# Kernel optimization log

Hardware: AMD Instinct MI355X
Metric: run time of the kernel (lower is better)

## Reference

```python
import jax, jax.numpy as jnp
import numpy as np

B, L, D, H = 2, 2048, 1024, 16
DH = D // H  # per-head dim = 64


def setup_inputs() -> dict:
    key = jax.random.key(0)
    ks = jax.random.split(key, 7)
    s = 1.0 / np.sqrt(D)
    x = jax.random.normal(ks[0], (B, L, D), dtype=jnp.float32)
    Wq = jax.random.normal(ks[1], (D, D), dtype=jnp.float32) * s
    bq = jax.random.normal(ks[2], (D,), dtype=jnp.float32) * s
    Wk = jax.random.normal(ks[3], (D, D), dtype=jnp.float32) * s
    bk = jax.random.normal(ks[4], (D,), dtype=jnp.float32) * s
    Wv = jax.random.normal(ks[5], (D, D), dtype=jnp.float32) * s
    bv = jax.random.normal(ks[6], (D,), dtype=jnp.float32) * s
    # strict upper-triangular causal mask; mask==1 means position is masked (-inf)
    atten_mask = jnp.triu(jnp.ones((L, L), dtype=jnp.int32), k=1)
    return {"x": x, "atten_mask": atten_mask, "Wq": Wq, "bq": bq,
            "Wk": Wk, "bk": bk, "Wv": Wv, "bv": bv}


def reference(x, atten_mask, Wq, bq, Wk, bk, Wv, bv):
    # nn.Linear: y = x @ W^T + b
    q = x @ Wq.T + bq  # [B,L,D]
    k = x @ Wk.T + bk
    v = x @ Wv.T + bv
    # contiguous split into heads == reshape to [B,L,H,DH]
    q = q.reshape(B, L, H, DH)
    k = k.reshape(B, L, H, DH)
    v = v.reshape(B, L, H, DH)
    scale = jnp.sqrt(jnp.float32(DH))
    scores = jnp.einsum('blhd,bmhd->bhlm', q, k) / scale  # [B,H,L,L]
    # torch.where(mask == 1, -inf, scores)
    scores = jnp.where(atten_mask[None, None] == 1, -jnp.inf, scores)
    attn = jax.nn.softmax(scores, axis=-1)
    out = jnp.einsum('bhlm,bmhd->blhd', attn, v)  # [B,L,H,DH]
    return out.reshape(B, L, D)  # concat heads along channel dim
```

## Files before the change

### kernel.cpp

```cpp
#include <hip/hip_runtime.h>
#include <hip/hip_bf16.h>

#define BDIM 2
#define LSEQ 2048
#define DMODEL 1024
#define NH 16
#define DHEAD 64
#define SP 72
#define CTS 136

typedef __bf16 bf16_t;
typedef __attribute__((ext_vector_type(8))) __bf16 bf16x8;
typedef __attribute__((ext_vector_type(4))) __bf16 bf16x4;
typedef __attribute__((ext_vector_type(2))) __bf16 bf16x2;
typedef __attribute__((ext_vector_type(4))) float f32x4;
typedef __attribute__((ext_vector_type(4))) int i32x4;

static __device__ __forceinline__ f32x4 mfma16(bf16x8 a, bf16x8 b, f32x4 c) {
    return __builtin_amdgcn_mfma_f32_16x16x32_bf16(a, b, c, 0, 0, 0);
}

static __device__ __forceinline__ void load_lds16(const bf16_t* g, void* l) {
    __builtin_amdgcn_global_load_lds(
        (const __attribute__((address_space(1))) void*)g,
        (__attribute__((address_space(3))) void*)l, 16, 0, 0);
}

__global__ void convert_all(
    const float* __restrict__ x,
    const float* __restrict__ Wq, const float* __restrict__ Wk, const float* __restrict__ Wv,
    const float* __restrict__ bq, const float* __restrict__ bk, const float* __restrict__ bv,
    bf16_t* __restrict__ cx,
    bf16_t* __restrict__ cWq, bf16_t* __restrict__ cWk, bf16_t* __restrict__ cWv,
    bf16_t* __restrict__ cbq, bf16_t* __restrict__ cbk, bf16_t* __restrict__ cbv,
    float SQ)
{
    const int blk = blockIdx.x;
    const float* src; bf16_t* dst; int base, cnt; float sc = 1.0f;
    if (blk < 1024)      { src = x;  dst = cx;  base = blk * 1024;          cnt = 1024; }
    else if (blk < 1280) { src = Wq; dst = cWq; base = (blk - 1024) * 1024; cnt = 1024; sc = SQ; }
    else if (blk < 1536) { src = Wk; dst = cWk; base = (blk - 1280) * 1024; cnt = 1024; }
    else if (blk < 1792) { src = Wv; dst = cWv; base = (blk - 1536) * 1024; cnt = 1024; }
    else if (blk == 1792){ src = bq; dst = cbq; base = 0; cnt = 256; sc = SQ; }
    else if (blk == 1793){ src = bk; dst = cbk; base = 0; cnt = 256; }
    else                 { src = bv; dst = cbv; base = 0; cnt = 256; }

    for (int i = base + threadIdx.x; i < base + cnt; i += 256) {
        f32x4 v = *(const f32x4*)(src + 4 * (size_t)i);
        bf16x4 o;
        o[0] = (bf16_t)(v[0] * sc); o[1] = (bf16_t)(v[1] * sc);
        o[2] = (bf16_t)(v[2] * sc); o[3] = (bf16_t)(v[3] * sc);
        *(bf16x4*)(dst + 4 * (size_t)i) = o;
    }
}

__global__ __launch_bounds__(256) void qkv_gemm(
    const bf16_t* __restrict__ x,
    const bf16_t* __restrict__ W0, const bf16_t* __restrict__ W1, const bf16_t* __restrict__ W2,
    const bf16_t* __restrict__ b0, const bf16_t* __restrict__ b1, const bf16_t* __restrict__ b2,
    bf16_t* __restrict__ yq, bf16_t* __restrict__ yk, bf16_t* __restrict__ yvT)
{
    __shared__ alignas(16) bf16_t smem[2 * 16384];
    bf16_t* Ct = smem;

    const int tid  = threadIdx.x;
    const int lane = tid & 63;
    const int w    = tid >> 6;
    const int quad = lane >> 4;
    const int n16  = lane & 15;

    const int m0 = blockIdx.y * 128;
    const int n0 = blockIdx.x * 128;
    const int z  = blockIdx.z;

    const bf16_t* W    = (z == 0) ? W0 : ((z == 1) ? W1 : W2);
    const bf16_t* bias = (z == 0) ? b0 : ((z == 1) ? b1 : b2);

    const int wm = (w >> 1) * 64;
    const int wn = (w & 1) * 64;

    f32x4 acc[4][4] = {};

    const int srow  = lane >> 3;
    const int schnk = (lane & 7) ^ srow;
    const bf16_t* gx = x + (size_t)(m0 + w * 32 + srow) * DMODEL + schnk * 8;
    const bf16_t* gw = W + (size_t)(n0 + w * 32 + srow) * DMODEL + schnk * 8;
    const int dOff = w * 2048;

    const int swz = n16 & 7;

    {
        bf16_t* lA = smem + dOff;
        bf16_t* lB = smem + 8192 + dOff;
        #pragma unroll
        for (int ii = 0; ii < 4; ++ii) {
            load_lds16(gx + (size_t)(8 * ii) * DMODEL, lA + ii * 512);
            load_lds16(gw + (size_t)(8 * ii) * DMODEL, lB + ii * 512);
        }
    }
    __syncthreads();

    int buf = 0;
    for (int it = 0; it < 16; ++it) {
        if (it + 1 < 16) {
            const int k0 = (it + 1) * 64;
            bf16_t* lA = smem + (buf ^ 1) * 16384 + dOff;
            bf16_t* lB = smem + (buf ^ 1) * 16384 + 8192 + dOff;
            #pragma unroll
            for (int ii = 0; ii < 4; ++ii) {
                load_lds16(gx + (size_t)(8 * ii) * DMODEL + k0, lA + ii * 512);
                load_lds16(gw + (size_t)(8 * ii) * DMODEL + k0, lB + ii * 512);
            }
        }

        const bf16_t* Ab = smem + buf * 16384;
        const bf16_t* Bb = smem + buf * 16384 + 8192;
        #pragma unroll
        for (int kk = 0; kk < 2; ++kk) {
            bf16x8 af[4], bfv[4];
            #pragma unroll
            for (int mt = 0; mt < 4; ++mt) {
                const bf16_t* ar = Ab + (wm + mt * 16 + n16) * 64;
                af[mt] = *(const bf16x8*)(ar + ((quad + 4 * kk) ^ swz) * 8);
            }
            #pragma unroll
            for (int nt = 0; nt < 4; ++nt) {
                const bf16_t* br = Bb + (wn + nt * 16 + n16) * 64;
                bfv[nt] = *(const bf16x8*)(br + ((quad + 4 * kk) ^ swz) * 8);
            }
            #pragma unroll
            for (int mt = 0; mt < 4; ++mt)
                #pragma unroll
                for (int nt = 0; nt < 4; ++nt)
                    acc[mt][nt] = mfma16(af[mt], bfv[nt], acc[mt][nt]);
        }

        __syncthreads();
        buf ^= 1;
    }

    if (z < 2) {
        bf16_t* y = (z == 0) ? yq : yk;
        #pragma unroll
        for (int nt = 0; nt < 4; ++nt) {
            int jc = wn + nt * 16 + n16;
            float bv = (float)bias[n0 + jc];
            #pragma unroll
            for (int mt = 0; mt < 4; ++mt) {
                int rr = wm + mt * 16 + quad * 4;
                #pragma unroll
                for (int r = 0; r < 4; ++r)
                    Ct[(rr + r) * CTS + jc] = (bf16_t)(acc[mt][nt][r] + bv);
            }
        }
        __syncthreads();
        const int l    = tid >> 1;
        const int half = tid & 1;
        const int hh   = (n0 >> 6) + half;
        const int i    = m0 + l;
        const int bb   = i >> 11, ll = i & 2047;
        bf16_t* dst = &y[(((size_t)bb * NH + hh) * LSEQ + ll) * DHEAD];
        const bf16_t* srcr = &Ct[l * CTS + half * 64];
        #pragma unroll
        for (int c = 0; c < 8; ++c)
            *(bf16x8*)(dst + c * 8) = *(const bf16x8*)(srcr + c * 8);
    } else {
        #pragma unroll
        for (int nt = 0; nt < 4; ++nt) {
            int j = n0 + wn + nt * 16 + n16;
            float bv = (float)bias[j];
            #pragma unroll
            for (int mt = 0; mt < 4; ++mt) {
                int i0 = m0 + wm + mt * 16 + quad * 4;
                int bb = i0 >> 11, l = i0 & 2047;
                bf16x4 pk;
                #pragma unroll
                for (int r = 0; r < 4; ++r) pk[r] = (bf16_t)(acc[mt][nt][r] + bv);
                *(bf16x4*)(&yvT[((size_t)bb * DMODEL + j) * LSEQ + l]) = pk;
            }
        }
    }
}

__global__ __launch_bounds__(256) void attn_fused(
    const bf16_t* __restrict__ qp,
    const bf16_t* __restrict__ kp,
    const bf16_t* __restrict__ vtp,
    float* __restrict__ out,
    float* __restrict__ Opart,
    float* __restrict__ ml)
{
    __shared__ alignas(16) bf16_t Ks[2][64 * 64];
    __shared__ alignas(16) bf16_t Vs[2][64 * 64];
    __shared__ alignas(16) bf16_t Pw[4][2][32 * SP];

    const int tid  = threadIdx.x;
    const int lane = tid & 63;
    const int w    = tid >> 6;
    const int quad = lane >> 4;
    const int n16  = lane & 15;
    const int lane3 = lane >> 3;
    const int lane7 = lane & 7;
    const int swz8  = (lane7 ^ lane3) * 8;
    const int swz   = n16 & 7;

    const int bh  = blockIdx.x;
    const int yy  = blockIdx.y;
    const int p   = yy & 7;
    const bool isA = (yy < 8);
    const int b = bh >> 4, h = bh & 15;
    const size_t hb = (size_t)bh * (LSEQ * DHEAD);

    float l_[2];
    f32x4 oacc[2][4];

    auto process = [&](int qt, int t0, int ntiles, bool maskTail) {
        int iqg[2];
        bf16x8 qb[2][2];
        #pragma unroll
        for (int g = 0; g < 2; ++g) {
            iqg[g] = qt * 128 + 32 * w + 16 * g + n16;
            const bf16_t* qq = qp + hb + (size_t)iqg[g] * DHEAD;
            qb[g][0] = *(const bf16x8*)(qq + quad * 8);
            qb[g][1] = *(const bf16x8*)(qq + 32 + quad * 8);
        }

        const bf16_t* gk = kp  + hb + (size_t)(t0 * 64 + 16 * w + lane3) * DHEAD + swz8;
        const bf16_t* gv = vtp + hb + (size_t)(16 * w + lane3) * LSEQ + t0 * 64 + swz8;

        int buf = 0;
        {
            char* lk = (char*)&Ks[0][0] + w * 2048;
            char* lv = (char*)&Vs[0][0] + w * 2048;
            load_lds16(gk,             lk);
            load_lds16(gk + 8 * DHEAD, lk + 1024);
            load_lds16(gv,             lv);
            load_lds16(gv + 8 * LSEQ,  lv + 1024);
            gk += 64 * DHEAD; gv += 64;
        }
        __syncthreads();

        for (int it = 0; it < ntiles; ++it) {
            if (it + 1 < ntiles) {
                char* lk = (char*)&Ks[buf ^ 1][0] + w * 2048;
                char* lv = (char*)&Vs[buf ^ 1][0] + w * 2048;
                load_lds16(gk,             lk);
                load_lds16(gk + 8 * DHEAD, lk + 1024);
                load_lds16(gv,             lv);
                load_lds16(gv + 8 * LSEQ,  lv + 1024);
                gk += 64 * DHEAD; gv += 64;
            }

            const bf16_t* kb = &Ks[buf][0];
            f32x4 s[2][4];
            #pragma unroll
            for (int t = 0; t < 4; ++t) {
                const bf16_t* krow = kb + (t * 16 + n16) * 64;
                bf16x8 k0v = *(const bf16x8*)(krow + ((quad    ) ^ swz) * 8);
                bf16x8 k1v = *(const bf16x8*)(krow + ((quad + 4) ^ swz) * 8);
                #pragma unroll
                for (int g = 0; g < 2; ++g) {
                    f32x4 z = {0.f, 0.f, 0.f, 0.f};
                    z = mfma16(k0v, qb[g][0], z);
                    z = mfma16(k1v, qb[g][1], z);
                    s[g][t] = z;
                }
            }

            if (maskTail && it >= ntiles - 2) {
                const int k0 = (t0 + it) * 64;
                #pragma unroll
                for (int g = 0; g < 2; ++g)
                    #pragma unroll
                    for (int t = 0; t < 4; ++t)
                        #pragma unroll
                        for (int r = 0; r < 4; ++r)
                            if (k0 + t * 16 + quad * 4 + r > iqg[g]) s[g][t][r] = -1e30f;
            }

            #pragma unroll
            for (int g = 0; g < 2; ++g) {
                bf16_t* pw = &Pw[w][buf][g * 16 * SP] + n16 * SP + quad * 4;
                float rs = 0.f;
                #pragma unroll
                for (int t = 0; t < 4; ++t) {
                    float p0 = __builtin_amdgcn_exp2f(s[g][t][0]);
                    float p1 = __builtin_amdgcn_exp2f(s[g][t][1]);
                    float p2 = __builtin_amdgcn_exp2f(s[g][t][2]);
                    float p3 = __builtin_amdgcn_exp2f(s[g][t][3]);
                    rs += (p0 + p1) + (p2 + p3);
                    bf16x4 pk;
                    pk[0] = (bf16_t)p0; pk[1] = (bf16_t)p1;
                    pk[2] = (bf16_t)p2; pk[3] = (bf16_t)p3;
                    *(bf16x4*)(pw + t * 16) = pk;
                }
                l_[g] += rs;
            }

            asm volatile("s_waitcnt lgkmcnt(0)" ::: "memory");

            const bf16_t* vbs = &Vs[buf][0];
            #pragma unroll
            for (int c = 0; c < 2; ++c) {
                bf16x8 pb0 = *(const bf16x8*)(&Pw[w][buf][0]       + n16 * SP + c * 32 + quad * 8);
                bf16x8 pb1 = *(const bf16x8*)(&Pw[w][buf][16 * SP] + n16 * SP + c * 32 + quad * 8);
                #pragma unroll
                for (int t = 0; t < 4; ++t) {
                    const bf16_t* vrow = vbs + (t * 16 + n16) * 64;
                    bf16x8 va = *(const bf16x8*)(vrow + ((quad + 4 * c) ^ swz) * 8);
                    oacc[0][t] = mfma16(va, pb0, oacc[0][t]);
                    oacc[1][t] = mfma16(va, pb1, oacc[1][t]);
                }
            }

            __syncthreads();
            buf ^= 1;
        }
    };

    auto zero_state = [&]() {
        #pragma unroll
        for (int g = 0; g < 2; ++g) {
            l_[g] = 0.f;
            #pragma unroll
            for (int t = 0; t < 4; ++t) { f32x4 zz = {0.f,0.f,0.f,0.f}; oacc[g][t] = zz; }
        }
    };

    auto store_partial = [&](int pidx) {
        #pragma unroll
        for (int g = 0; g < 2; ++g) {
            float ls = l_[g];
            ls += __shfl_xor(ls, 16, 64);
            ls += __shfl_xor(ls, 32, 64);
            const int row = 32 * w + 16 * g + n16;
            float* Ob = Opart + (size_t)pidx * (128 * 64) + row * 64;
            #pragma unroll
            for (int t = 0; t < 4; ++t)
                *(f32x4*)(Ob + t * 16 + quad * 4) = oacc[g][t];
            if (quad == 0) ml[(size_t)pidx * 128 + row] = ls;
        }
    };

    if (isA) {
        zero_state();
        process(p, 0, 2 * p + 2, true);
        #pragma unroll
        for (int g = 0; g < 2; ++g) {
            float ls = l_[g];
            ls += __shfl_xor(ls, 16, 64);
            ls += __shfl_xor(ls, 32, 64);
            const float inv = 1.0f / ls;
            const int iq = p * 128 + 32 * w + 16 * g + n16;
            float* orow = out + ((size_t)b * LSEQ + iq) * DMODEL + h * DHEAD;
            #pragma unroll
            for (int t = 0; t < 4; ++t) {
                f32x4 o;
                o[0] = oacc[g][t][0] * inv; o[1] = oacc[g][t][1] * inv;
                o[2] = oacc[g][t][2] * inv; o[3] = oacc[g][t][3] * inv;
                *(f32x4*)(orow + t * 16 + quad * 4) = o;
            }
        }
        zero_state();
        process(15 - p, 0, 15 - 2 * p, false);
        store_partial((bh * 8 + (7 - p)) * 2 + 0);
    } else {
        zero_state();
        process(15 - p, 15 - 2 * p, 17, true);
        store_partial((bh * 8 + (7 - p)) * 2 + 1);
    }
}

__global__ __launch_bounds__(256) void attn_combine(
    const float* __restrict__ Opart, const float* __restrict__ ml,
    float* __restrict__ out)
{
    const int bh = blockIdx.x;
    const int q8 = blockIdx.y;
    const int t  = threadIdx.x;
    const int row = t >> 1;
    const int dh0 = (t & 1) * 32;
    const int p0  = (bh * 8 + q8) * 2;
    const int b = bh >> 4, h = bh & 15;

    float l0 = ml[(size_t)p0 * 128 + row];
    float l1 = ml[(size_t)(p0 + 1) * 128 + row];
    float inv = 1.0f / (l0 + l1);

    const float* P0 = Opart + (size_t)p0 * (128 * 64) + row * 64 + dh0;
    const float* P1 = P0 + 128 * 64;
    float* orow = out + ((size_t)b * LSEQ + ((8 + q8) * 128 + row)) * DMODEL
                + h * DHEAD + dh0;
    #pragma unroll
    for (int c = 0; c < 8; ++c) {
        f32x4 o0 = *(const f32x4*)(P0 + 4 * c);
        f32x4 o1 = *(const f32x4*)(P1 + 4 * c);
        f32x4 o;
        o[0] = (o0[0] + o1[0]) * inv;
        o[1] = (o0[1] + o1[1]) * inv;
        o[2] = (o0[2] + o1[2]) * inv;
        o[3] = (o0[3] + o1[3]) * inv;
        *(f32x4*)(orow + 4 * c) = o;
    }
}

extern "C" void kernel_launch(void* const* d_in, const int* in_sizes, int n_in,
                              void* d_out, int out_size, void* d_ws, size_t ws_size,
                              hipStream_t stream)
{
    const float* x  = (const float*)d_in[0];
    const float* Wq = (const float*)d_in[2];
    const float* bq = (const float*)d_in[3];
    const float* Wk = (const float*)d_in[4];
    const float* bk = (const float*)d_in[5];
    const float* Wv = (const float*)d_in[6];
    const float* bv = (const float*)d_in[7];
    float* out = (float*)d_out;

    char* ws = (char*)d_ws;
    bf16_t* q   = (bf16_t*)(ws);
    bf16_t* k   = (bf16_t*)(ws + 8u  * 1024 * 1024);
    bf16_t* vT  = (bf16_t*)(ws + 16u * 1024 * 1024);
    bf16_t* cx  = (bf16_t*)(ws + 24u * 1024 * 1024);
    bf16_t* cWq = (bf16_t*)(ws + 32u * 1024 * 1024);
    bf16_t* cWk = (bf16_t*)(ws + 34u * 1024 * 1024);
    bf16_t* cWv = (bf16_t*)(ws + 36u * 1024 * 1024);
    bf16_t* cbq = (bf16_t*)(ws + 38u * 1024 * 1024);
    bf16_t* cbk = (bf16_t*)(ws + 38u * 1024 * 1024 + 4096);
    bf16_t* cbv = (bf16_t*)(ws + 38u * 1024 * 1024 + 8192);
    float*  mlp = (float*) (ws + 39u * 1024 * 1024);
    float*  Op  = (float*) (ws + 40u * 1024 * 1024);

    const float SQ = 0.125f * 1.44269504088896f;

    convert_all<<<1795, 256, 0, stream>>>(x, Wq, Wk, Wv, bq, bk, bv,
                                          cx, cWq, cWk, cWv, cbq, cbk, cbv, SQ);

    dim3 g1(DMODEL / 128, (BDIM * LSEQ) / 128, 3);
    qkv_gemm<<<g1, 256, 0, stream>>>(cx, cWq, cWk, cWv, cbq, cbk, cbv, q, k, vT);

    dim3 g2(BDIM * NH, 16, 1);
    attn_fused<<<g2, 256, 0, stream>>>(q, k, vT, out, Op, mlp);

    dim3 g3(BDIM * NH, 8, 1);
    attn_combine<<<g3, 256, 0, stream>>>(Op, mlp, out);
}
```

Before: 174.8 us.

## Restructure QKV GEMM into 256x256 tiles with 8 waves and interleaved async staging

The QKV projection GEMM moves from 128x128 tiles with 4 waves to 256x256 tiles with 8 waves and 128KB of LDS. The k-loop is split into quarter phases that interleave global-to-LDS loads for the next A tile and the B tile two steps ahead with MFMA bursts. These phases use explicit barriers, waitcnt, sched_barrier and setprio. The grid shrinks to 192 blocks with a swizzled tile order for L2 locality. This targets more operand reuse per LDS load and better memory/compute overlap, at the cost of fewer blocks on the GPU and tricky hand synchronisation.

```diff
diff --git a/kernel.cpp b/kernel.cpp
--- a/kernel.cpp
+++ b/kernel.cpp
@@ -54,125 +54,167 @@
     }
 }
 
-__global__ __launch_bounds__(256) void qkv_gemm(
+__global__ __launch_bounds__(512, 2) void qkv_gemm(
     const bf16_t* __restrict__ x,
     const bf16_t* __restrict__ W0, const bf16_t* __restrict__ W1, const bf16_t* __restrict__ W2,
     const bf16_t* __restrict__ b0, const bf16_t* __restrict__ b1, const bf16_t* __restrict__ b2,
     bf16_t* __restrict__ yq, bf16_t* __restrict__ yk, bf16_t* __restrict__ yvT)
 {
-    __shared__ alignas(16) bf16_t smem[2 * 16384];
-    bf16_t* Ct = smem;
+    __shared__ alignas(16) bf16_t smem[65536];
 
     const int tid  = threadIdx.x;
     const int lane = tid & 63;
     const int w    = tid >> 6;
     const int quad = lane >> 4;
     const int n16  = lane & 15;
-
-    const int m0 = blockIdx.y * 128;
-    const int n0 = blockIdx.x * 128;
-    const int z  = blockIdx.z;
+    const int swz  = n16 & 7;
+    const int srow = lane >> 3;
+    const int schnk = (lane & 7) ^ srow;
+
+    const int s   = blockIdx.x;
+    const int sem = ((s & 7) << 3) | (s >> 3);
+    const int m0  = (sem >> 2) * 256;
+    const int n0  = (sem & 3) * 256;
+    const int z   = blockIdx.y;
 
     const bf16_t* W    = (z == 0) ? W0 : ((z == 1) ? W1 : W2);
     const bf16_t* bias = (z == 0) ? b0 : ((z == 1) ? b1 : b2);
 
-    const int wm = (w >> 1) * 64;
-    const int wn = (w & 1) * 64;
-
-    f32x4 acc[4][4] = {};
-
-    const int srow  = lane >> 3;
-    const int schnk = (lane & 7) ^ srow;
-    const bf16_t* gx = x + (size_t)(m0 + w * 32 + srow) * DMODEL + schnk * 8;
-    const bf16_t* gw = W + (size_t)(n0 + w * 32 + srow) * DMODEL + schnk * 8;
-    const int dOff = w * 2048;
-
-    const int swz = n16 & 7;
-
-    {
-        bf16_t* lA = smem + dOff;
-        bf16_t* lB = smem + 8192 + dOff;
-        #pragma unroll
-        for (int ii = 0; ii < 4; ++ii) {
-            load_lds16(gx + (size_t)(8 * ii) * DMODEL, lA + ii * 512);
-            load_lds16(gw + (size_t)(8 * ii) * DMODEL, lB + ii * 512);
-        }
-    }
-    __syncthreads();
-
-    int buf = 0;
-    for (int it = 0; it < 16; ++it) {
-        if (it + 1 < 16) {
-            const int k0 = (it + 1) * 64;
-            bf16_t* lA = smem + (buf ^ 1) * 16384 + dOff;
-            bf16_t* lB = smem + (buf ^ 1) * 16384 + 8192 + dOff;
-            #pragma unroll
-            for (int ii = 0; ii < 4; ++ii) {
-                load_lds16(gx + (size_t)(8 * ii) * DMODEL + k0, lA + ii * 512);
-                load_lds16(gw + (size_t)(8 * ii) * DMODEL + k0, lB + ii * 512);
-            }
-        }
-
-        const bf16_t* Ab = smem + buf * 16384;
-        const bf16_t* Bb = smem + buf * 16384 + 8192;
-        #pragma unroll
-        for (int kk = 0; kk < 2; ++kk) {
-            bf16x8 af[4], bfv[4];
-            #pragma unroll
-            for (int mt = 0; mt < 4; ++mt) {
-                const bf16_t* ar = Ab + (wm + mt * 16 + n16) * 64;
-                af[mt] = *(const bf16x8*)(ar + ((quad + 4 * kk) ^ swz) * 8);
-            }
+    const int wm = (w >> 2) * 128;
+    const int wn = (w & 3) * 64;
+
+    const bf16_t* gA = x + (size_t)(m0 + w * 8 + srow) * DMODEL + schnk * 8;
+    const bf16_t* gB = W + (size_t)(n0 + w * 8 + srow) * DMODEL + schnk * 8;
+
+    f32x4 acc[8][4] = {};
+
+    auto stageA = [&](int buf, int h, int kt) {
+        bf16_t* d = smem + buf * 32768 + (h * 128 + w * 8) * 64;
+        const bf16_t* src = gA + (size_t)(h * 128) * DMODEL + kt * 64;
+        load_lds16(src, d);
+        load_lds16(src + (size_t)64 * DMODEL, d + 64 * 64);
+    };
+    auto stageB = [&](int buf, int h, int kt) {
+        bf16_t* d = smem + buf * 32768 + 16384 + (h * 128 + w * 8) * 64;
+        const bf16_t* src = gB + (size_t)(h * 128) * DMODEL + kt * 64;
+        load_lds16(src, d);
+        load_lds16(src + (size_t)64 * DMODEL, d + 64 * 64);
+    };
+
+    stageA(0, 0, 0); stageA(0, 1, 0);
+    stageB(0, 0, 0); stageB(0, 1, 0);
+    stageB(1, 0, 1); stageB(1, 1, 1);
+    asm volatile("s_waitcnt vmcnt(4)" ::: "memory");
+    __builtin_amdgcn_s_barrier();
+
+    for (int u = 0; u < 16; ++u) {
+        const int buf = u & 1;
+        const bf16_t* Ab = smem + buf * 32768;
+        const bf16_t* Bb = Ab + 16384;
+
+        bf16x8 bfr[4][2], af[2][2];
+        #pragma unroll
+        for (int nt = 0; nt < 4; ++nt) {
+            const bf16_t* br = Bb + (wn + nt * 16 + n16) * 64;
+            bfr[nt][0] = *(const bf16x8*)(br + ((quad    ) ^ swz) * 8);
+            bfr[nt][1] = *(const bf16x8*)(br + ((quad + 4) ^ swz) * 8);
+        }
+        #pragma unroll
+        for (int m2 = 0; m2 < 2; ++m2) {
+            const bf16_t* ar = Ab + (wm + m2 * 16 + n16) * 64;
+            af[m2][0] = *(const bf16x8*)(ar + ((quad    ) ^ swz) * 8);
+            af[m2][1] = *(const bf16x8*)(ar + ((quad + 4) ^ swz) * 8);
+        }
+        if (u + 1 < 16) stageA(buf ^ 1, 0, u + 1);
+        __builtin_amdgcn_s_barrier();
+        asm volatile("s_waitcnt lgkmcnt(0)" ::: "memory");
+        __builtin_amdgcn_sched_barrier(0);
+        __builtin_amdgcn_s_setprio(1);
+        #pragma unroll
+        for (int m2 = 0; m2 < 2; ++m2)
             #pragma unroll
             for (int nt = 0; nt < 4; ++nt) {
-                const bf16_t* br = Bb + (wn + nt * 16 + n16) * 64;
-                bfv[nt] = *(const bf16x8*)(br + ((quad + 4 * kk) ^ swz) * 8);
-            }
-            #pragma unroll
-            for (int mt = 0; mt < 4; ++mt)
-                #pragma unroll
-                for (int nt = 0; nt < 4; ++nt)
-                    acc[mt][nt] = mfma16(af[mt], bfv[nt], acc[mt][nt]);
-        }
-
-        __syncthreads();
-        buf ^= 1;
+                acc[m2][nt] = mfma16(af[m2][0], bfr[nt][0], acc[m2][nt]);
+                acc[m2][nt] = mfma16(af[m2][1], bfr[nt][1], acc[m2][nt]);
+            }
+        __builtin_amdgcn_s_setprio(0);
+        __builtin_amdgcn_s_barrier();
+
+        #pragma unroll
+        for (int q = 1; q < 4; ++q) {
+            #pragma unroll
+            for (int m2 = 0; m2 < 2; ++m2) {
+                const bf16_t* ar = Ab + (wm + (2 * q + m2) * 16 + n16) * 64;
+                af[m2][0] = *(const bf16x8*)(ar + ((quad    ) ^ swz) * 8);
+                af[m2][1] = *(const bf16x8*)(ar + ((quad + 4) ^ swz) * 8);
+            }
+            if (q == 1) {
+                if (u + 1 < 16) stageA(buf ^ 1, 1, u + 1);
+                if (u + 2 < 16) stageB(buf, 0, u + 2);
+            } else if (q == 2) {
+                if (u + 2 < 16) stageB(buf, 1, u + 2);
+            }
+            __builtin_amdgcn_s_barrier();
+            asm volatile("s_waitcnt lgkmcnt(0)" ::: "memory");
+            __builtin_amdgcn_sched_barrier(0);
+            __builtin_amdgcn_s_setprio(1);
+            #pragma unroll
+            for (int m2 = 0; m2 < 2; ++m2)
+                #pragma unroll
+                for (int nt = 0; nt < 4; ++nt) {
+                    acc[2 * q + m2][nt] = mfma16(af[m2][0], bfr[nt][0], acc[2 * q + m2][nt]);
+                    acc[2 * q + m2][nt] = mfma16(af[m2][1], bfr[nt][1], acc[2 * q + m2][nt]);
+                }
+            __builtin_amdgcn_s_setprio(0);
+            if (q == 3) {
+                if (u < 14) asm volatile("s_waitcnt vmcnt(4)" ::: "memory");
+                else        asm volatile("s_waitcnt vmcnt(0)" ::: "memory");
+            }
+            __builtin_amdgcn_s_barrier();
+        }
     }
 
     if (z < 2) {
         bf16_t* y = (z == 0) ? yq : yk;
+        bf16_t* Ct = smem;
+        #pragma unroll
+        for (int hp = 0; hp < 2; ++hp) {
+            if (((w & 3) >> 1) == hp) {
+                #pragma unroll
+                for (int nt = 0; nt < 4; ++nt) {
+                    const int jc = (w & 1) * 64 + nt * 16 + n16;
+                    const float bv = (float)bias[n0 + hp * 128 + jc];
+                    #pragma unroll
+                    for (int mt = 0; mt < 8; ++mt) {
+                        const int rr = wm + mt * 16 + quad * 4;
+                        #pragma unroll
+                        for (int r = 0; r < 4; ++r)
+                            Ct[(rr + r) * CTS + jc] = (bf16_t)(acc[mt][nt][r] + bv);
+                    }
+                }
+            }
+            __syncthreads();
+            const int row = tid >> 1;
+            const int seg = tid & 1;
+            const int hh  = (n0 >> 6) + hp * 2 + seg;
+            const int i   = m0 + row;
+            const int bb  = i >> 11, ll = i & 2047;
+            bf16_t* dst = &y[(((size_t)bb * NH + hh) * LSEQ + ll) * DHEAD];
+            const bf16_t* srcr = &Ct[row * CTS + seg * 64];
+            #pragma unroll
+            for (int c = 0; c < 8; ++c)
+                *(bf16x8*)(dst + c * 8) = *(const bf16x8*)(srcr + c * 8);
+            __syncthreads();
+        }
+    } else {
         #pragma unroll
         for (int nt = 0; nt < 4; ++nt) {
-            int jc = wn + nt * 16 + n16;
-            float bv = (float)bias[n0 + jc];
-            #pragma unroll
-            for (int mt = 0; mt < 4; ++mt) {
-                int rr = wm + mt * 16 + quad * 4;
-                #pragma unroll
-                for (int r = 0; r < 4; ++r)
-                    Ct[(rr + r) * CTS + jc] = (bf16_t)(acc[mt][nt][r] + bv);
-            }
-        }
-        __syncthreads();
-        const int l    = tid >> 1;
-        const int half = tid & 1;
-        const int hh   = (n0 >> 6) + half;
-        const int i    = m0 + l;
-        const int bb   = i >> 11, ll = i & 2047;
-        bf16_t* dst = &y[(((size_t)bb * NH + hh) * LSEQ + ll) * DHEAD];
-        const bf16_t* srcr = &Ct[l * CTS + half * 64];
-        #pragma unroll
-        for (int c = 0; c < 8; ++c)
-            *(bf16x8*)(dst + c * 8) = *(const bf16x8*)(srcr + c * 8);
-    } else {
-        #pragma unroll
-        for (int nt = 0; nt < 4; ++nt) {
-            int j = n0 + wn + nt * 16 + n16;
-            float bv = (float)bias[j];
-            #pragma unroll
-            for (int mt = 0; mt < 4; ++mt) {
-                int i0 = m0 + wm + mt * 16 + quad * 4;
-                int bb = i0 >> 11, l = i0 & 2047;
+            const int j = n0 + wn + nt * 16 + n16;
+            const float bv = (float)bias[j];
+            #pragma unroll
+            for (int mt = 0; mt < 8; ++mt) {
+                const int i0 = m0 + wm + mt * 16 + quad * 4;
+                const int bb = i0 >> 11, l = i0 & 2047;
                 bf16x4 pk;
                 #pragma unroll
                 for (int r = 0; r < 4; ++r) pk[r] = (bf16_t)(acc[mt][nt][r] + bv);
@@ -436,8 +478,8 @@
     convert_all<<<1795, 256, 0, stream>>>(x, Wq, Wk, Wv, bq, bk, bv,
                                           cx, cWq, cWk, cWv, cbq, cbk, cbv, SQ);
 
-    dim3 g1(DMODEL / 128, (BDIM * LSEQ) / 128, 3);
-    qkv_gemm<<<g1, 256, 0, stream>>>(cx, cWq, cWk, cWv, cbq, cbk, cbv, q, k, vT);
+    dim3 g1(64, 3, 1);
+    qkv_gemm<<<g1, 512, 0, stream>>>(cx, cWq, cWk, cWv, cbq, cbk, cbv, q, k, vT);
 
     dim3 g2(BDIM * NH, 16, 1);
     attn_fused<<<g2, 256, 0, stream>>>(q, k, vT, out, Op, mlp);
```

New measurement: 174.8 us. Within noise of the previous version (+0.0%).
